# Kernel optimization log

Hardware: AMD Instinct MI355X
Metric: run time of the kernel (lower is better)

Reference implementation:

```python
import jax, jax.numpy as jnp
import numpy as np
import math

B, S, DIM = 2, 2048, 2048
H = 16
NOPE, ROPE = 96, 32
HD = 128          # head_dim = NOPE + ROPE
KVR, QR = 512, 1536


def _rope_tables():
    inv_freq = 1.0 / (10000.0 ** (np.arange(0, ROPE, 2, dtype=np.float32) / ROPE))  # [ROPE/2]
    t = np.arange(S, dtype=np.float32)
    freqs = np.outer(t, inv_freq)  # [S, ROPE/2]
    return jnp.asarray(np.cos(freqs)), jnp.asarray(np.sin(freqs))


def setup_inputs() -> dict:
    key = jax.random.key(0)
    ks = jax.random.split(key, 8)
    w = 0.02
    cos, sin = _rope_tables()
    return {
        "x": jax.random.normal(ks[0], (B, S, DIM), jnp.float32),
        "freqs_cos": cos,
        "freqs_sin": sin,
        "wq_down": jax.random.normal(ks[1], (DIM, QR), jnp.float32) * w,
        "wq_up": jax.random.normal(ks[2], (QR, H * HD), jnp.float32) * w,
        "wkv_down": jax.random.normal(ks[3], (DIM, KVR), jnp.float32) * w,
        "w_up_nope": jax.random.normal(ks[4], (KVR, H * NOPE), jnp.float32) * w,
        "w_up_rope": jax.random.normal(ks[5], (KVR, H * ROPE), jnp.float32) * w,
        "w_up_val": jax.random.normal(ks[6], (KVR, H * HD), jnp.float32) * w,
        "wo": jax.random.normal(ks[7], (H * HD, DIM), jnp.float32) * w,
    }


def _apply_rope(x, cos, sin):
    # x: [B, S, H, D_r]; cos/sin: [S, D_r/2]
    xr = x[..., 0::2]
    xi = x[..., 1::2]
    c = cos[None, :, None, :]
    s = sin[None, :, None, :]
    out_r = xr * c - xi * s
    out_i = xr * s + xi * c
    return jnp.stack([out_r, out_i], axis=-1).reshape(x.shape)


def reference(x, freqs_cos, freqs_sin, wq_down, wq_up, wkv_down,
              w_up_nope, w_up_rope, w_up_val, wo):
    b, s, _ = x.shape
    # Q path: low-rank down then up
    q = (x @ wq_down) @ wq_up                 # [B,S,H*HD]
    q = q.reshape(b, s, H, HD)
    q_nope, q_rope = q[..., :NOPE], q[..., NOPE:]
    q_rope = _apply_rope(q_rope, freqs_cos, freqs_sin)

    # KV path: shared latent
    kv_latent = x @ wkv_down                  # [B,S,KVR]
    k_nope = (kv_latent @ w_up_nope).reshape(b, s, H, NOPE)
    k_rope = _apply_rope((kv_latent @ w_up_rope).reshape(b, s, H, ROPE),
                         freqs_cos, freqs_sin)
    v = (kv_latent @ w_up_val).reshape(b, s, H, HD)

    q_final = jnp.concatenate([q_nope, q_rope], axis=-1)   # [B,S,H,HD]
    k_final = jnp.concatenate([k_nope, k_rope], axis=-1)

    scores = jnp.einsum("bqhd,bkhd->bhqk", q_final, k_final) / math.sqrt(HD)
    causal = jnp.tril(jnp.ones((s, s), dtype=bool))        # [S,S]
    scores = jnp.where(causal[None, None], scores, -jnp.inf)
    attn = jax.nn.softmax(scores, axis=-1)
    out = jnp.einsum("bhqk,bkhd->bqhd", attn, v).reshape(b, s, H * HD)
    return out @ wo
```

## Files before the change

### kernel.cpp

```cpp
#include <hip/hip_runtime.h>
#include <hip/hip_bf16.h>
#include <stdint.h>

#define B_    2
#define S_    2048
#define DIM_  2048
#define H_    16
#define NOPE_ 96
#define ROPE_ 32
#define HD_   128
#define KVR_  512
#define QR_   1536
#define BS_   (B_*S_)
#define NQT_  (S_/128)

typedef __bf16 bf16_t;
typedef bf16_t bf16x8 __attribute__((ext_vector_type(8)));
typedef float  f32x4  __attribute__((ext_vector_type(4)));

__device__ __forceinline__ uint16_t f2bf(float f) {
  union { float f; uint32_t u; } v; v.f = f;
  uint32_t r = (v.u + 0x7fffu + ((v.u >> 16) & 1u)) >> 16;
  return (uint16_t)r;
}
__device__ __forceinline__ float bf2f(uint16_t h) {
  union { uint32_t u; float f; } v; v.u = ((uint32_t)h) << 16;
  return v.f;
}

__device__ __forceinline__ void gl_lds16(const void* g, void* l) {
  __builtin_amdgcn_global_load_lds(
      (const __attribute__((address_space(1))) uint32_t*)g,
      (__attribute__((address_space(3))) uint32_t*)l, 16, 0, 0);
}

__global__ __launch_bounds__(256) void cast_bf16_k(const float* __restrict__ X,
                                                   uint16_t* __restrict__ Y, int n) {
  int i = (blockIdx.x * 256 + threadIdx.x) * 4;
  if (i + 3 < n) {
    float4 v = *(const float4*)&X[i];
    ushort4 o; o.x = f2bf(v.x); o.y = f2bf(v.y); o.z = f2bf(v.z); o.w = f2bf(v.w);
    *(ushort4*)&Y[i] = o;
  }
}

__global__ __launch_bounds__(256) void transpose_cast_k(const float* __restrict__ W,
                                                        uint16_t* __restrict__ Wt,
                                                        int K, int N, float scale) {
  __shared__ __align__(16) float tile[64][65];
  const int n0 = blockIdx.x * 64, k0 = blockIdx.y * 64;
  const int tid = threadIdx.x;
  #pragma unroll
  for (int i = 0; i < 4; i++) {
    int p = i * 256 + tid;
    int r = p >> 4, c4 = (p & 15) * 4;
    float4 v = *(const float4*)&W[(size_t)(k0 + r) * N + n0 + c4];
    tile[r][c4 + 0] = v.x; tile[r][c4 + 1] = v.y; tile[r][c4 + 2] = v.z; tile[r][c4 + 3] = v.w;
  }
  __syncthreads();
  #pragma unroll
  for (int i = 0; i < 4; i++) {
    int p = i * 256 + tid;
    int rn = p >> 4, c4 = (p & 15) * 4;
    ushort4 o;
    o.x = f2bf(tile[c4 + 0][rn] * scale); o.y = f2bf(tile[c4 + 1][rn] * scale);
    o.z = f2bf(tile[c4 + 2][rn] * scale); o.w = f2bf(tile[c4 + 3][rn] * scale);
    *(ushort4*)&Wt[(size_t)(n0 + rn) * K + k0 + c4] = o;
  }
}

template<int STORE_F32>
__global__ __launch_bounds__(256) void gemm_bt(const uint16_t* __restrict__ A,
                                               const uint16_t* __restrict__ Bt,
                                               void* __restrict__ C,
                                               int M, int N, int K,
                                               int lda, int ldb, int ldc) {
  __shared__ __align__(16) uint16_t As[128][64];
  __shared__ __align__(16) uint16_t Bs[128][64];
  const int tid = threadIdx.x;
  const int wave = tid >> 6, lane = tid & 63;
  const int wm = wave & 1, wn = wave >> 1;
  const int m0 = blockIdx.y * 128, n0 = blockIdx.x * 128;
  const int fr = lane & 15, fq = lane >> 4;

  f32x4 acc[4][4] = {};

  const int srow = wave * 32 + (lane >> 3);
  const int sg   = ((lane & 7) ^ ((lane >> 3) & 7));
  const int scol = sg * 8;

  for (int k0 = 0; k0 < K; k0 += 64) {
    #pragma unroll
    for (int i = 0; i < 4; i++) {
      gl_lds16(A  + (size_t)(m0 + srow + i * 8) * lda + k0 + scol, &As[wave * 32 + i * 8][0]);
      gl_lds16(Bt + (size_t)(n0 + srow + i * 8) * ldb + k0 + scol, &Bs[wave * 32 + i * 8][0]);
    }
    __syncthreads();
    #pragma unroll
    for (int ks = 0; ks < 2; ks++) {
      bf16x8 af[4], bf[4];
      #pragma unroll
      for (int mt = 0; mt < 4; mt++) {
        int pc = (ks * 4 + fq) ^ (fr & 7);
        af[mt] = *(const bf16x8*)&As[wm * 64 + mt * 16 + fr][pc * 8];
      }
      #pragma unroll
      for (int nt = 0; nt < 4; nt++) {
        int pc = (ks * 4 + fq) ^ (fr & 7);
        bf[nt] = *(const bf16x8*)&Bs[wn * 64 + nt * 16 + fr][pc * 8];
      }
      #pragma unroll
      for (int mt = 0; mt < 4; mt++)
        #pragma unroll
        for (int nt = 0; nt < 4; nt++)
          acc[mt][nt] = __builtin_amdgcn_mfma_f32_16x16x32_bf16(af[mt], bf[nt], acc[mt][nt], 0, 0, 0);
    }
    __syncthreads();
  }
  #pragma unroll
  for (int mt = 0; mt < 4; mt++) {
    #pragma unroll
    for (int nt = 0; nt < 4; nt++) {
      #pragma unroll
      for (int r = 0; r < 4; r++) {
        int gm = m0 + wm * 64 + mt * 16 + fq * 4 + r;
        int gn = n0 + wn * 64 + nt * 16 + fr;
        if (STORE_F32) ((float*)C)[(size_t)gm * ldc + gn] = acc[mt][nt][r];
        else          ((uint16_t*)C)[(size_t)gm * ldc + gn] = f2bf(acc[mt][nt][r]);
      }
    }
  }
}

__global__ __launch_bounds__(256) void rope_assemble_k(uint16_t* __restrict__ q,
                                                       const uint16_t* __restrict__ kcat,
                                                       uint16_t* __restrict__ k_final,
                                                       const float* __restrict__ cos_t,
                                                       const float* __restrict__ sin_t) {
  const int row = blockIdx.x;
  const int s = row & (S_ - 1);
  const int tid = threadIdx.x;
  const uint16_t* kr = kcat + (size_t)row * 2048;
  #pragma unroll
  for (int it = 0; it < 4; it++) {
    int p = it * 256 + tid;
    int hh = p >> 6;
    int j = p & 63;
    int d = 2 * j;
    if (d < NOPE_) {
      uint32_t val = *(const uint32_t*)&kr[hh * NOPE_ + d];
      *(uint32_t*)&k_final[(size_t)row * (H_ * HD_) + hh * HD_ + d] = val;
    } else {
      int i = (d - NOPE_) >> 1;
      float c = cos_t[s * (ROPE_ / 2) + i], sn = sin_t[s * (ROPE_ / 2) + i];
      const uint16_t* krp = kr + 1536 + hh * ROPE_ + (d - NOPE_);
      float xr = bf2f(krp[0]), xi = bf2f(krp[1]);
      size_t kfi = (size_t)row * (H_ * HD_) + hh * HD_ + d;
      k_final[kfi]     = f2bf(xr * c - xi * sn);
      k_final[kfi + 1] = f2bf(xr * sn + xi * c);
      size_t qi = (size_t)row * (H_ * HD_) + hh * HD_ + d;
      float qr = bf2f(q[qi]), qi2 = bf2f(q[qi + 1]);
      q[qi]     = f2bf(qr * c - qi2 * sn);
      q[qi + 1] = f2bf(qr * sn + qi2 * c);
    }
  }
}

__global__ __launch_bounds__(512) void attn_kernel(const uint16_t* __restrict__ Q,
                                                   const uint16_t* __restrict__ Kf,
                                                   const uint16_t* __restrict__ Vt,
                                                   uint16_t* __restrict__ O) {
  __shared__ __align__(16) uint16_t Ks[64][128];
  __shared__ __align__(16) uint16_t Vs[128][64];
  __shared__ __align__(16) uint16_t Ps[8][16][72];
  const int bid = blockIdx.x;
  const int qt = (NQT_ - 1) - (bid / (H_ * B_));
  const int hb = bid % (H_ * B_);
  const int h = hb >> 1, b = hb & 1;
  const int tid = threadIdx.x, wave = tid >> 6, lane = tid & 63;
  const int fr = lane & 15, fq = lane >> 4;
  const int q0 = qt * 128;
  const int qrow = q0 + wave * 16;

  bf16x8 qf[4];
  const uint16_t* qbase = Q + (size_t)(b * S_ + qrow + fr) * (H_ * HD_) + h * HD_ + fq * 8;
  #pragma unroll
  for (int s4 = 0; s4 < 4; s4++) qf[s4] = *(const bf16x8*)(qbase + s4 * 32);

  float l_r[4] = {0.f, 0.f, 0.f, 0.f};
  f32x4 oacc[8] = {};

  const int ksrow_lo = wave * 4 + (lane >> 4);
  const int kg_chunk0 = (lane & 15);
  const int vsrow_lo = wave * 8 + (lane >> 3);
  const int vg_chunk = (lane & 7) ^ ((lane >> 3) & 7);

  const int nkt = 2 * qt + 2;
  for (int kt = 0; kt < nkt; kt++) {
    #pragma unroll
    for (int i = 0; i < 2; i++) {
      int row = i * 32 + ksrow_lo;
      int g = kg_chunk0 ^ (row & 15);
      gl_lds16(Kf + (size_t)(b * S_ + kt * 64 + row) * (H_ * HD_) + h * HD_ + g * 8,
               &Ks[i * 32 + wave * 4][0]);
    }
    #pragma unroll
    for (int i = 0; i < 2; i++) {
      int row = i * 64 + vsrow_lo;
      gl_lds16(Vt + (size_t)(h * HD_ + row) * BS_ + b * S_ + kt * 64 + vg_chunk * 8,
               &Vs[i * 64 + wave * 8][0]);
    }
    __syncthreads();

    if (kt * 64 <= qrow + 15) {
      f32x4 sacc[4] = {};
      #pragma unroll
      for (int ks = 0; ks < 4; ks++) {
        int pc = (ks * 4 + fq) ^ fr;
        #pragma unroll
        for (int nt = 0; nt < 4; nt++) {
          bf16x8 kfr = *(const bf16x8*)&Ks[nt * 16 + fr][pc * 8];
          sacc[nt] = __builtin_amdgcn_mfma_f32_16x16x32_bf16(qf[ks], kfr, sacc[nt], 0, 0, 0);
        }
      }
      const bool need_mask = (kt * 64 + 63 > qrow);
      #pragma unroll
      for (int nt = 0; nt < 4; nt++) {
        #pragma unroll
        for (int r = 0; r < 4; r++) {
          float p = __expf(sacc[nt][r]);
          if (need_mask) {
            int kg = kt * 64 + nt * 16 + fr;
            int qg = qrow + fq * 4 + r;
            if (kg > qg) p = 0.f;
          }
          l_r[r] += p;
          Ps[wave][fq * 4 + r][nt * 16 + fr] = f2bf(p);
        }
      }
      #pragma unroll
      for (int ks = 0; ks < 2; ks++) {
        bf16x8 pf = *(const bf16x8*)&Ps[wave][fr][ks * 32 + fq * 8];
        int pc = (ks * 4 + fq) ^ (fr & 7);
        #pragma unroll
        for (int d = 0; d < 8; d++) {
          bf16x8 vf = *(const bf16x8*)&Vs[d * 16 + fr][pc * 8];
          oacc[d] = __builtin_amdgcn_mfma_f32_16x16x32_bf16(pf, vf, oacc[d], 0, 0, 0);
        }
      }
    }
    __syncthreads();
  }
  #pragma unroll
  for (int mm = 1; mm < 16; mm <<= 1) {
    #pragma unroll
    for (int r = 0; r < 4; r++) l_r[r] += __shfl_xor(l_r[r], mm);
  }
  float inv_l[4];
  #pragma unroll
  for (int r = 0; r < 4; r++) inv_l[r] = 1.0f / l_r[r];
  #pragma unroll
  for (int d = 0; d < 8; d++) {
    #pragma unroll
    for (int r = 0; r < 4; r++) {
      int gm = b * S_ + qrow + fq * 4 + r;
      int gn = h * HD_ + d * 16 + fr;
      O[(size_t)gm * (H_ * HD_) + gn] = f2bf(oacc[d][r] * inv_l[r]);
    }
  }
}

extern "C" void kernel_launch(void* const* d_in, const int* in_sizes, int n_in,
                              void* d_out, int out_size, void* d_ws, size_t ws_size,
                              hipStream_t stream) {
  const float* x        = (const float*)d_in[0];
  const float* fcos     = (const float*)d_in[1];
  const float* fsin     = (const float*)d_in[2];
  const float* wq_down  = (const float*)d_in[3];
  const float* wq_up    = (const float*)d_in[4];
  const float* wkv_down = (const float*)d_in[5];
  const float* w_nope   = (const float*)d_in[6];
  const float* w_rope   = (const float*)d_in[7];
  const float* w_val    = (const float*)d_in[8];
  const float* wo       = (const float*)d_in[9];
  float* out = (float*)d_out;

  char* ws = (char*)d_ws;
  size_t off = 0;
  auto alloc = [&](size_t elems) {
    uint16_t* p = (uint16_t*)(ws + off);
    off += elems * 2; off = (off + 255) & ~(size_t)255;
    return p;
  };
  uint16_t* xb     = alloc((size_t)BS_ * DIM_);
  uint16_t* wdT    = alloc((size_t)(QR_ + KVR_) * DIM_);
  uint16_t* wquT   = alloc((size_t)(H_ * HD_) * QR_);
  uint16_t* wkrT   = alloc((size_t)(H_ * NOPE_ + H_ * ROPE_) * KVR_);
  uint16_t* wvT    = alloc((size_t)(H_ * HD_) * KVR_);
  uint16_t* woT    = alloc((size_t)DIM_ * (H_ * HD_));
  uint16_t* latcat = alloc((size_t)BS_ * (QR_ + KVR_));
  uint16_t* qbuf   = alloc((size_t)BS_ * (H_ * HD_));
  uint16_t* kcat   = alloc((size_t)BS_ * 2048);
  uint16_t* kfin   = alloc((size_t)BS_ * (H_ * HD_));
  uint16_t* vTb    = alloc((size_t)(H_ * HD_) * BS_);
  uint16_t* aout   = alloc((size_t)BS_ * (H_ * HD_));

  const float qscale = 0.08838834764831845f;

  cast_bf16_k<<<dim3((BS_ * DIM_) / 1024), 256, 0, stream>>>(x, xb, BS_ * DIM_);
  transpose_cast_k<<<dim3(QR_ / 64, DIM_ / 64), 256, 0, stream>>>(wq_down, wdT, DIM_, QR_, 1.f);
  transpose_cast_k<<<dim3(KVR_ / 64, DIM_ / 64), 256, 0, stream>>>(wkv_down, wdT + (size_t)QR_ * DIM_, DIM_, KVR_, 1.f);
  transpose_cast_k<<<dim3((H_ * HD_) / 64, QR_ / 64), 256, 0, stream>>>(wq_up, wquT, QR_, H_ * HD_, qscale);
  transpose_cast_k<<<dim3((H_ * NOPE_) / 64, KVR_ / 64), 256, 0, stream>>>(w_nope, wkrT, KVR_, H_ * NOPE_, 1.f);
  transpose_cast_k<<<dim3((H_ * ROPE_) / 64, KVR_ / 64), 256, 0, stream>>>(w_rope, wkrT + (size_t)(H_ * NOPE_) * KVR_, KVR_, H_ * ROPE_, 1.f);
  transpose_cast_k<<<dim3((H_ * HD_) / 64, KVR_ / 64), 256, 0, stream>>>(w_val, wvT, KVR_, H_ * HD_, 1.f);
  transpose_cast_k<<<dim3((H_ * HD_) / 64, DIM_ / 64), 256, 0, stream>>>(wo, woT, DIM_, H_ * HD_, 1.f);

  gemm_bt<0><<<dim3(2048 / 128, BS_ / 128), 256, 0, stream>>>(xb, wdT, latcat,
      BS_, 2048, DIM_, DIM_, DIM_, 2048);
  gemm_bt<0><<<dim3((H_ * HD_) / 128, BS_ / 128), 256, 0, stream>>>(latcat, wquT, qbuf,
      BS_, H_ * HD_, QR_, 2048, QR_, H_ * HD_);
  gemm_bt<0><<<dim3(2048 / 128, BS_ / 128), 256, 0, stream>>>(latcat + QR_, wkrT, kcat,
      BS_, 2048, KVR_, 2048, KVR_, 2048);
  gemm_bt<0><<<dim3(BS_ / 128, (H_ * HD_) / 128), 256, 0, stream>>>(wvT, latcat + QR_, vTb,
      H_ * HD_, BS_, KVR_, KVR_, 2048, BS_);

  rope_assemble_k<<<dim3(BS_), 256, 0, stream>>>(qbuf, kcat, kfin, fcos, fsin);
  attn_kernel<<<dim3(NQT_ * H_ * B_), 512, 0, stream>>>(qbuf, kfin, vTb, aout);
  gemm_bt<1><<<dim3(DIM_ / 128, BS_ / 128), 256, 0, stream>>>(aout, woT, out,
      BS_, DIM_, DIM_, DIM_, DIM_, DIM_);
}
```

Before: 375.4 us.

## Merge prep kernels, fuse RoPE into GEMM epilogues, transpose attention MFMA layout

Merges the x cast and all weight transpose-casts into a single prep kernel, which cuts seven launches. The RoPE rotation and the K head reassembly move into the Q and K up-projection GEMM epilogues via a lane shuffle, so the separate rope kernel and the kcat round-trip are gone. The attention kernel swaps MFMA operand order so each lane holds a single query row. P tiles can then be written with packed bf16 stores, the row-sum needs only two shuffles, and the output is stored as ushort4. The risks are a heavier GEMM epilogue with scattered cos/sin loads and added branch divergence inside the merged prep kernel.

Result: no change. 371.6 us (-1.0%).

```diff
diff --git a/kernel.cpp b/kernel.cpp
--- a/kernel.cpp
+++ b/kernel.cpp
@@ -27,6 +27,12 @@
   union { uint32_t u; float f; } v; v.u = ((uint32_t)h) << 16;
   return v.f;
 }
+__device__ __forceinline__ uint32_t pk_bf16(float a, float b) {
+  union { float f; uint32_t u; } x, y; x.f = a; y.f = b;
+  uint32_t lo = (x.u + 0x7fffu + ((x.u >> 16) & 1u)) >> 16;
+  uint32_t hi = (y.u + 0x7fffu + ((y.u >> 16) & 1u)) & 0xffff0000u;
+  return hi | lo;
+}
 
 __device__ __forceinline__ void gl_lds16(const void* g, void* l) {
   __builtin_amdgcn_global_load_lds(
@@ -34,21 +40,12 @@
       (__attribute__((address_space(3))) uint32_t*)l, 16, 0, 0);
 }
 
-__global__ __launch_bounds__(256) void cast_bf16_k(const float* __restrict__ X,
-                                                   uint16_t* __restrict__ Y, int n) {
-  int i = (blockIdx.x * 256 + threadIdx.x) * 4;
-  if (i + 3 < n) {
-    float4 v = *(const float4*)&X[i];
-    ushort4 o; o.x = f2bf(v.x); o.y = f2bf(v.y); o.z = f2bf(v.z); o.w = f2bf(v.w);
-    *(ushort4*)&Y[i] = o;
-  }
-}
-
-__global__ __launch_bounds__(256) void transpose_cast_k(const float* __restrict__ W,
-                                                        uint16_t* __restrict__ Wt,
-                                                        int K, int N, float scale) {
-  __shared__ __align__(16) float tile[64][65];
-  const int n0 = blockIdx.x * 64, k0 = blockIdx.y * 64;
+__device__ __forceinline__ void transpose_tile(const float* __restrict__ W,
+                                               uint16_t* __restrict__ Wt,
+                                               int K, int N, float scale, int lbid,
+                                               float (*tile)[65]) {
+  const int nb = N / 64;
+  const int n0 = (lbid % nb) * 64, k0 = (lbid / nb) * 64;
   const int tid = threadIdx.x;
   #pragma unroll
   for (int i = 0; i < 4; i++) {
@@ -69,12 +66,48 @@
   }
 }
 
-template<int STORE_F32>
+#define CAST_BLKS 2048
+__global__ __launch_bounds__(256) void prep_k(
+    const float* __restrict__ x,
+    const float* __restrict__ wqd, const float* __restrict__ wqu,
+    const float* __restrict__ wkvd, const float* __restrict__ wn,
+    const float* __restrict__ wr, const float* __restrict__ wv,
+    const float* __restrict__ wo,
+    uint16_t* __restrict__ xb, uint16_t* __restrict__ wdT,
+    uint16_t* __restrict__ wquT, uint16_t* __restrict__ wkrT,
+    uint16_t* __restrict__ wvT, uint16_t* __restrict__ woT, float qscale) {
+  __shared__ __align__(16) float tile[64][65];
+  int bid = blockIdx.x;
+  const int tid = threadIdx.x;
+  if (bid < CAST_BLKS) {
+    #pragma unroll
+    for (int p = 0; p < 4; p++) {
+      int i = bid * 4096 + p * 1024 + tid * 4;
+      float4 v = *(const float4*)&x[i];
+      ushort4 o; o.x = f2bf(v.x); o.y = f2bf(v.y); o.z = f2bf(v.z); o.w = f2bf(v.w);
+      *(ushort4*)&xb[i] = o;
+    }
+    return;
+  }
+  bid -= CAST_BLKS;
+  if (bid < 768)               transpose_tile(wqd,  wdT,                        2048, 1536, 1.f,    bid, tile);
+  else if ((bid -= 768) < 256) transpose_tile(wkvd, wdT + (size_t)QR_ * DIM_,   2048,  512, 1.f,    bid, tile);
+  else if ((bid -= 256) < 768) transpose_tile(wqu,  wquT,                       1536, 2048, qscale, bid, tile);
+  else if ((bid -= 768) < 192) transpose_tile(wn,   wkrT,                        512, 1536, 1.f,    bid, tile);
+  else if ((bid -= 192) < 64)  transpose_tile(wr,   wkrT + (size_t)1536 * 512,   512,  512, 1.f,    bid, tile);
+  else if ((bid -= 64) < 256)  transpose_tile(wv,   wvT,                         512, 2048, 1.f,    bid, tile);
+  else                         transpose_tile(wo,   woT, 2048, 2048, 1.f, bid - 256, tile);
+}
+#define PREP_BLKS (CAST_BLKS + 768 + 256 + 768 + 192 + 64 + 256 + 1024)
+
+template<int MODE>
 __global__ __launch_bounds__(256) void gemm_bt(const uint16_t* __restrict__ A,
                                                const uint16_t* __restrict__ Bt,
                                                void* __restrict__ C,
                                                int M, int N, int K,
-                                               int lda, int ldb, int ldc) {
+                                               int lda, int ldb, int ldc,
+                                               const float* __restrict__ cos_t,
+                                               const float* __restrict__ sin_t) {
   __shared__ __align__(16) uint16_t As[128][64];
   __shared__ __align__(16) uint16_t Bs[128][64];
   const int tid = threadIdx.x;
@@ -125,43 +158,38 @@
       for (int r = 0; r < 4; r++) {
         int gm = m0 + wm * 64 + mt * 16 + fq * 4 + r;
         int gn = n0 + wn * 64 + nt * 16 + fr;
-        if (STORE_F32) ((float*)C)[(size_t)gm * ldc + gn] = acc[mt][nt][r];
-        else          ((uint16_t*)C)[(size_t)gm * ldc + gn] = f2bf(acc[mt][nt][r]);
-      }
-    }
-  }
-}
-
-__global__ __launch_bounds__(256) void rope_assemble_k(uint16_t* __restrict__ q,
-                                                       const uint16_t* __restrict__ kcat,
-                                                       uint16_t* __restrict__ k_final,
-                                                       const float* __restrict__ cos_t,
-                                                       const float* __restrict__ sin_t) {
-  const int row = blockIdx.x;
-  const int s = row & (S_ - 1);
-  const int tid = threadIdx.x;
-  const uint16_t* kr = kcat + (size_t)row * 2048;
-  #pragma unroll
-  for (int it = 0; it < 4; it++) {
-    int p = it * 256 + tid;
-    int hh = p >> 6;
-    int j = p & 63;
-    int d = 2 * j;
-    if (d < NOPE_) {
-      uint32_t val = *(const uint32_t*)&kr[hh * NOPE_ + d];
-      *(uint32_t*)&k_final[(size_t)row * (H_ * HD_) + hh * HD_ + d] = val;
-    } else {
-      int i = (d - NOPE_) >> 1;
-      float c = cos_t[s * (ROPE_ / 2) + i], sn = sin_t[s * (ROPE_ / 2) + i];
-      const uint16_t* krp = kr + 1536 + hh * ROPE_ + (d - NOPE_);
-      float xr = bf2f(krp[0]), xi = bf2f(krp[1]);
-      size_t kfi = (size_t)row * (H_ * HD_) + hh * HD_ + d;
-      k_final[kfi]     = f2bf(xr * c - xi * sn);
-      k_final[kfi + 1] = f2bf(xr * sn + xi * c);
-      size_t qi = (size_t)row * (H_ * HD_) + hh * HD_ + d;
-      float qr = bf2f(q[qi]), qi2 = bf2f(q[qi + 1]);
-      q[qi]     = f2bf(qr * c - qi2 * sn);
-      q[qi + 1] = f2bf(qr * sn + qi2 * c);
+        float v = acc[mt][nt][r];
+        if (MODE == 0) {
+          ((uint16_t*)C)[(size_t)gm * ldc + gn] = f2bf(v);
+        } else if (MODE == 1) {
+          ((float*)C)[(size_t)gm * ldc + gn] = v;
+        } else if (MODE == 2) {
+          float other = __shfl_xor(v, 1);
+          int d = gn & 127;
+          if (d >= 96) {
+            int s = gm & (S_ - 1);
+            int i = (d - 96) >> 1;
+            float c = cos_t[s * 16 + i], sn = sin_t[s * 16 + i];
+            v = (fr & 1) ? (other * sn + v * c) : (v * c - other * sn);
+          }
+          ((uint16_t*)C)[(size_t)gm * ldc + gn] = f2bf(v);
+        } else {
+          float other = __shfl_xor(v, 1);
+          int dstcol;
+          if (gn < 1536) {
+            int h = gn / 96;
+            dstcol = h * 128 + (gn - h * 96);
+          } else {
+            int ln = gn - 1536;
+            int h = ln >> 5, dd = ln & 31;
+            int s = gm & (S_ - 1);
+            float c = cos_t[s * 16 + (dd >> 1)], sn = sin_t[s * 16 + (dd >> 1)];
+            v = (fr & 1) ? (other * sn + v * c) : (v * c - other * sn);
+            dstcol = h * 128 + 96 + dd;
+          }
+          ((uint16_t*)C)[(size_t)gm * 2048 + dstcol] = f2bf(v);
+        }
+      }
     }
   }
 }
@@ -187,7 +215,7 @@
   #pragma unroll
   for (int s4 = 0; s4 < 4; s4++) qf[s4] = *(const bf16x8*)(qbase + s4 * 32);
 
-  float l_r[4] = {0.f, 0.f, 0.f, 0.f};
+  float l_s = 0.f;
   f32x4 oacc[8] = {};
 
   const int ksrow_lo = wave * 4 + (lane >> 4);
@@ -220,23 +248,26 @@
         #pragma unroll
         for (int nt = 0; nt < 4; nt++) {
           bf16x8 kfr = *(const bf16x8*)&Ks[nt * 16 + fr][pc * 8];
-          sacc[nt] = __builtin_amdgcn_mfma_f32_16x16x32_bf16(qf[ks], kfr, sacc[nt], 0, 0, 0);
+          sacc[nt] = __builtin_amdgcn_mfma_f32_16x16x32_bf16(kfr, qf[ks], sacc[nt], 0, 0, 0);
         }
       }
       const bool need_mask = (kt * 64 + 63 > qrow);
+      const int qg = qrow + fr;
       #pragma unroll
       for (int nt = 0; nt < 4; nt++) {
+        float p[4];
         #pragma unroll
         for (int r = 0; r < 4; r++) {
-          float p = __expf(sacc[nt][r]);
+          float pp = __expf(sacc[nt][r]);
           if (need_mask) {
-            int kg = kt * 64 + nt * 16 + fr;
-            int qg = qrow + fq * 4 + r;
-            if (kg > qg) p = 0.f;
+            int kg = kt * 64 + nt * 16 + fq * 4 + r;
+            if (kg > qg) pp = 0.f;
           }
-          l_r[r] += p;
-          Ps[wave][fq * 4 + r][nt * 16 + fr] = f2bf(p);
+          l_s += pp;
+          p[r] = pp;
         }
+        uint2 w; w.x = pk_bf16(p[0], p[1]); w.y = pk_bf16(p[2], p[3]);
+        *(uint2*)&Ps[wave][fr][nt * 16 + fq * 4] = w;
       }
       #pragma unroll
       for (int ks = 0; ks < 2; ks++) {
@@ -245,28 +276,22 @@
         #pragma unroll
         for (int d = 0; d < 8; d++) {
           bf16x8 vf = *(const bf16x8*)&Vs[d * 16 + fr][pc * 8];
-          oacc[d] = __builtin_amdgcn_mfma_f32_16x16x32_bf16(pf, vf, oacc[d], 0, 0, 0);
+          oacc[d] = __builtin_amdgcn_mfma_f32_16x16x32_bf16(vf, pf, oacc[d], 0, 0, 0);
         }
       }
     }
     __syncthreads();
   }
-  #pragma unroll
-  for (int mm = 1; mm < 16; mm <<= 1) {
-    #pragma unroll
-    for (int r = 0; r < 4; r++) l_r[r] += __shfl_xor(l_r[r], mm);
-  }
-  float inv_l[4];
-  #pragma unroll
-  for (int r = 0; r < 4; r++) inv_l[r] = 1.0f / l_r[r];
-  #pragma unroll
-  for (int d = 0; d < 8; d++) {
-    #pragma unroll
-    for (int r = 0; r < 4; r++) {
-      int gm = b * S_ + qrow + fq * 4 + r;
-      int gn = h * HD_ + d * 16 + fr;
-      O[(size_t)gm * (H_ * HD_) + gn] = f2bf(oacc[d][r] * inv_l[r]);
-    }
+  l_s += __shfl_xor(l_s, 16);
+  l_s += __shfl_xor(l_s, 32);
+  const float inv_l = 1.0f / l_s;
+  const int gm = b * S_ + qrow + fr;
+  #pragma unroll
+  for (int dt = 0; dt < 8; dt++) {
+    ushort4 o;
+    o.x = f2bf(oacc[dt][0] * inv_l); o.y = f2bf(oacc[dt][1] * inv_l);
+    o.z = f2bf(oacc[dt][2] * inv_l); o.w = f2bf(oacc[dt][3] * inv_l);
+    *(ushort4*)&O[(size_t)gm * (H_ * HD_) + h * HD_ + dt * 16 + fq * 4] = o;
   }
 }
 
@@ -300,33 +325,25 @@
   uint16_t* woT    = alloc((size_t)DIM_ * (H_ * HD_));
   uint16_t* latcat = alloc((size_t)BS_ * (QR_ + KVR_));
   uint16_t* qbuf   = alloc((size_t)BS_ * (H_ * HD_));
-  uint16_t* kcat   = alloc((size_t)BS_ * 2048);
   uint16_t* kfin   = alloc((size_t)BS_ * (H_ * HD_));
   uint16_t* vTb    = alloc((size_t)(H_ * HD_) * BS_);
   uint16_t* aout   = alloc((size_t)BS_ * (H_ * HD_));
 
   const float qscale = 0.08838834764831845f;
 
-  cast_bf16_k<<<dim3((BS_ * DIM_) / 1024), 256, 0, stream>>>(x, xb, BS_ * DIM_);
-  transpose_cast_k<<<dim3(QR_ / 64, DIM_ / 64), 256, 0, stream>>>(wq_down, wdT, DIM_, QR_, 1.f);
-  transpose_cast_k<<<dim3(KVR_ / 64, DIM_ / 64), 256, 0, stream>>>(wkv_down, wdT + (size_t)QR_ * DIM_, DIM_, KVR_, 1.f);
-  transpose_cast_k<<<dim3((H_ * HD_) / 64, QR_ / 64), 256, 0, stream>>>(wq_up, wquT, QR_, H_ * HD_, qscale);
-  transpose_cast_k<<<dim3((H_ * NOPE_) / 64, KVR_ / 64), 256, 0, stream>>>(w_nope, wkrT, KVR_, H_ * NOPE_, 1.f);
-  transpose_cast_k<<<dim3((H_ * ROPE_) / 64, KVR_ / 64), 256, 0, stream>>>(w_rope, wkrT + (size_t)(H_ * NOPE_) * KVR_, KVR_, H_ * ROPE_, 1.f);
-  transpose_cast_k<<<dim3((H_ * HD_) / 64, KVR_ / 64), 256, 0, stream>>>(w_val, wvT, KVR_, H_ * HD_, 1.f);
-  transpose_cast_k<<<dim3((H_ * HD_) / 64, DIM_ / 64), 256, 0, stream>>>(wo, woT, DIM_, H_ * HD_, 1.f);
+  prep_k<<<dim3(PREP_BLKS), 256, 0, stream>>>(x, wq_down, wq_up, wkv_down, w_nope,
+      w_rope, w_val, wo, xb, wdT, wquT, wkrT, wvT, woT, qscale);
 
   gemm_bt<0><<<dim3(2048 / 128, BS_ / 128), 256, 0, stream>>>(xb, wdT, latcat,
-      BS_, 2048, DIM_, DIM_, DIM_, 2048);
-  gemm_bt<0><<<dim3((H_ * HD_) / 128, BS_ / 128), 256, 0, stream>>>(latcat, wquT, qbuf,
-      BS_, H_ * HD_, QR_, 2048, QR_, H_ * HD_);
-  gemm_bt<0><<<dim3(2048 / 128, BS_ / 128), 256, 0, stream>>>(latcat + QR_, wkrT, kcat,
-      BS_, 2048, KVR_, 2048, KVR_, 2048);
+      BS_, 2048, DIM_, DIM_, DIM_, 2048, nullptr, nullptr);
+  gemm_bt<2><<<dim3((H_ * HD_) / 128, BS_ / 128), 256, 0, stream>>>(latcat, wquT, qbuf,
+      BS_, H_ * HD_, QR_, 2048, QR_, H_ * HD_, fcos, fsin);
+  gemm_bt<3><<<dim3(2048 / 128, BS_ / 128), 256, 0, stream>>>(latcat + QR_, wkrT, kfin,
+      BS_, 2048, KVR_, 2048, KVR_, 2048, fcos, fsin);
   gemm_bt<0><<<dim3(BS_ / 128, (H_ * HD_) / 128), 256, 0, stream>>>(wvT, latcat + QR_, vTb,
-      H_ * HD_, BS_, KVR_, KVR_, 2048, BS_);
-
-  rope_assemble_k<<<dim3(BS_), 256, 0, stream>>>(qbuf, kcat, kfin, fcos, fsin);
+      H_ * HD_, BS_, KVR_, KVR_, 2048, BS_, nullptr, nullptr);
+
   attn_kernel<<<dim3(NQT_ * H_ * B_), 512, 0, stream>>>(qbuf, kfin, vTb, aout);
   gemm_bt<1><<<dim3(DIM_ / 128, BS_ / 128), 256, 0, stream>>>(aout, woT, out,
-      BS_, DIM_, DIM_, DIM_, DIM_, DIM_);
-}
+      BS_, DIM_, DIM_, DIM_, DIM_, DIM_, nullptr, nullptr);
+}
```
